# Performance work log

Hardware: AMD Instinct MI355X
Metric: run time of the kernel (lower is better)

## Reference

```python
import jax, jax.numpy as jnp
import numpy as np

B, L, D = 16, 1024, 768

def setup_inputs() -> dict:
    key = jax.random.key(0)
    k1, k2, k3, k4 = jax.random.split(key, 4)
    d_embedding = jax.random.normal(k1, (B, L, D), dtype=jnp.float32)
    d_mask = jax.random.randint(k2, (B, L), 0, 2) == 1
    W = jax.random.normal(k3, (D, D), dtype=jnp.float32) / np.sqrt(D)
    b = jax.random.normal(k4, (D,), dtype=jnp.float32) * 0.01
    return {"d_embedding": d_embedding, "d_mask": d_mask, "W": W, "b": b}

def reference(d_embedding, d_mask, W, b):
    # linear + relu projection: [B, L, D]
    p = jax.nn.relu(jnp.einsum('bld,de->ble', d_embedding, W.T) + b)
    # self-attention scores: [B, L, L]
    scores = jnp.einsum('bld,bmd->blm', p, p)
    # zero out the diagonal (multiply by (1 - eye))
    diag_off = 1.0 - jnp.eye(L, dtype=scores.dtype)
    scores = scores * diag_off[None, :, :]
    # mask padded key positions with -inf (columns)
    scores = jnp.where(d_mask[:, None, :], -jnp.inf, scores)
    # softmax over keys
    alpha = jax.nn.softmax(scores, axis=-1)  # [B, L, L]
    align_feature = jnp.einsum('blm,bmd->bld', alpha, d_embedding)
    return align_feature, alpha
```

## Files before the change

### kernel.cpp

```cpp
#include <hip/hip_runtime.h>
#include <math.h>

#define B_ 16
#define L_ 1024
#define D_ 768

typedef short bf16x8 __attribute__((ext_vector_type(8)));
typedef _Float16 half8 __attribute__((ext_vector_type(8)));
typedef float f32x4 __attribute__((ext_vector_type(4)));

__device__ __forceinline__ unsigned short f2bf(float x) {
  unsigned u = __float_as_uint(x);
  u = (u + 0x7FFFu + ((u >> 16) & 1u)) >> 16;
  return (unsigned short)u;
}
__device__ __forceinline__ float bf2f(unsigned short h) {
  return __uint_as_float(((unsigned)h) << 16);
}
__device__ __forceinline__ unsigned short f2h(float x) {
  union { _Float16 h; unsigned short u; } v;
  v.h = (_Float16)x;
  return v.u;
}

__global__ __launch_bounds__(256) void k_mask2(const void* __restrict__ mraw,
                                               int* __restrict__ canon,
                                               int* __restrict__ psum,
                                               int* __restrict__ kinfo) {
  __shared__ int flags[2];
  __shared__ int tsum[256];
  const int b = blockIdx.x;
  const int tid = threadIdx.x;
  if (tid < 2) flags[tid] = 0;
  __syncthreads();
  const unsigned* m32 = (const unsigned*)mraw;
  int gt = 0, oddnz = 0;
  for (int i = tid; i < 4096; i += 256) {
    unsigned v = m32[i];
    if (v > 1u) gt = 1;
    if ((i & 1) && v != 0u) oddnz = 1;
  }
  if (gt) atomicOr(&flags[0], 1);
  if (oddnz) atomicOr(&flags[1], 1);
  __syncthreads();
  const int mode = flags[0] ? 0 : (flags[1] ? 1 : 2);
  int v[4];
#pragma unroll
  for (int e = 0; e < 4; ++e) {
    const int i = b * L_ + tid * 4 + e;
    int mv;
    if (mode == 0)      mv = ((const unsigned char*)mraw)[i];
    else if (mode == 1) mv = ((const int*)mraw)[i];
    else                mv = (int)(((const long long*)mraw)[i] != 0);
    v[e] = (mv != 0);
    canon[i] = v[e];
  }
  const int vc = (1 - v[0]) + (1 - v[1]) + (1 - v[2]) + (1 - v[3]);
  tsum[tid] = vc;
  __syncthreads();
  for (int off = 1; off < 256; off <<= 1) {
    const int t = (tid >= off) ? tsum[tid - off] : 0;
    __syncthreads();
    tsum[tid] += t;
    __syncthreads();
  }
  int run = tsum[tid] - vc;
#pragma unroll
  for (int e = 0; e < 4; ++e) {
    psum[b * L_ + tid * 4 + e] = run;
    run += 1 - v[e];
  }
  if (tid == 255) {
    const int tot = tsum[255];
    kinfo[b] = (tot + 63) >> 6;
    kinfo[16 + b] = tot;
  }
}

__global__ __launch_bounds__(256) void k_prep16(const float* __restrict__ X,
                                                unsigned short* __restrict__ Xf,
                                                unsigned short* __restrict__ Xt,
                                                const int* __restrict__ psum,
                                                const int* __restrict__ canon,
                                                const int* __restrict__ kinfo) {
  __shared__ unsigned short t16[64][66];
  const int b = blockIdx.z;
  const int d0 = blockIdx.x * 64, m0 = blockIdx.y * 64;
  const int dd = threadIdx.x & 63, mq = threadIdx.x >> 6;
#pragma unroll
  for (int i = 0; i < 16; ++i) {
    const int m = mq * 16 + i;
    const size_t gidx = ((size_t)b * L_ + m0 + m) * D_ + d0 + dd;
    const unsigned short h = f2h(X[gidx]);
    Xf[gidx] = h;
    t16[dd][m] = h;
  }
  __syncthreads();
  const int mm = threadIdx.x & 63, dq = threadIdx.x >> 6;
  const int gm = m0 + mm;
  if (!canon[b * L_ + gm]) {
    const int j = psum[b * L_ + gm];
#pragma unroll
    for (int i = 0; i < 16; ++i) {
      const int d = dq * 16 + i;
      Xt[((size_t)b * D_ + d0 + d) * L_ + j] = t16[d][mm];
    }
  }
  if (blockIdx.y == 15) {
    const int nt64 = kinfo[b] * 64;
    const int kv = kinfo[16 + b];
    if (kv < nt64) {
      const int rr = threadIdx.x >> 2, cg = threadIdx.x & 3;
      unsigned short* base = Xt + ((size_t)b * D_ + d0 + rr) * L_;
#pragma unroll
      for (int q = 0; q < 16; ++q) {
        const int c = kv + cg * 16 + q;
        if (c < nt64) base[c] = 0;
      }
    }
  }
}

__global__ __launch_bounds__(256) void k_prep(const float* __restrict__ X,
                                              unsigned short* __restrict__ Xh,
                                              unsigned short* __restrict__ Xl,
                                              unsigned short* __restrict__ Xt) {
  __shared__ unsigned short t16[64][66];
  const int b = blockIdx.z;
  const int d0 = blockIdx.x * 64, m0 = blockIdx.y * 64;
  const int dd = threadIdx.x & 63, mq = threadIdx.x >> 6;
#pragma unroll
  for (int i = 0; i < 16; ++i) {
    const int m = mq * 16 + i;
    const size_t gidx = ((size_t)b * L_ + m0 + m) * D_ + d0 + dd;
    const float x = X[gidx];
    const unsigned short h = f2bf(x);
    Xh[gidx] = h;
    Xl[gidx] = f2bf(x - bf2f(h));
    t16[dd][m] = h;
  }
  __syncthreads();
  const int mm = threadIdx.x & 63, dq = threadIdx.x >> 6;
#pragma unroll
  for (int i = 0; i < 16; ++i) {
    const int d = dq * 16 + i;
    Xt[((size_t)b * D_ + d0 + d) * L_ + m0 + mm] = t16[d][mm];
  }
}

__global__ __launch_bounds__(256) void k_castW(const float* __restrict__ W,
                                               unsigned short* __restrict__ Wf,
                                               int n8) {
  const int i = blockIdx.x * 256 + threadIdx.x;
  if (i >= n8) return;
  const float4 a = *(const float4*)(W + (size_t)i * 8);
  const float4 b = *(const float4*)(W + (size_t)i * 8 + 4);
  *(ushort4*)(Wf + (size_t)i * 8)     = make_ushort4(f2h(a.x), f2h(a.y), f2h(a.z), f2h(a.w));
  *(ushort4*)(Wf + (size_t)i * 8 + 4) = make_ushort4(f2h(b.x), f2h(b.y), f2h(b.z), f2h(b.w));
}

__device__ __forceinline__ void stage_panel(const unsigned short* __restrict__ ph,
                                            const unsigned short* __restrict__ pl,
                                            size_t grow0, int kk,
                                            char* ldsbase, int wave, int lane) {
#pragma unroll
  for (int q = 0; q < 4; ++q) {
    const int s = wave * 4 + q;
    const int row = s * 8 + (lane >> 3);
    const int xs = (lane & 7) ^ (row & 7);
    const unsigned short* src = (xs & 4) ? pl : ph;
    const unsigned short* g = src + (grow0 + row) * D_ + kk + (xs & 3) * 8;
    __builtin_amdgcn_global_load_lds(
        (const __attribute__((address_space(1))) void*)g,
        (__attribute__((address_space(3))) void*)(ldsbase + s * 1024),
        16, 0, 0);
  }
}

__device__ __forceinline__ void stage_panel1(const unsigned short* __restrict__ g0,
                                             size_t rstride,
                                             char* ldsbase, int wave, int lane) {
#pragma unroll
  for (int q = 0; q < 4; ++q) {
    const int s = wave * 4 + q;
    const int row = s * 8 + (lane >> 3);
    const int xs = (lane & 7) ^ (row & 7);
    const unsigned short* g = g0 + (size_t)row * rstride + xs * 8;
    __builtin_amdgcn_global_load_lds(
        (const __attribute__((address_space(1))) void*)g,
        (__attribute__((address_space(3))) void*)(ldsbase + s * 1024),
        16, 0, 0);
  }
}

__device__ __forceinline__ bf16x8 ldsfrag(const char* base, int row, int g) {
  return *(const bf16x8*)(base + row * 128 + ((g ^ (row & 7)) * 16));
}
__device__ __forceinline__ half8 ldsfrag_h(const char* base, int row, int g) {
  return *(const half8*)(base + row * 128 + ((g ^ (row & 7)) * 16));
}

__global__ __launch_bounds__(256) void k_proj3(const unsigned short* __restrict__ Xf,
                                               const unsigned short* __restrict__ Wf,
                                               const float* __restrict__ bias,
                                               unsigned short* __restrict__ Pf) {
  __shared__ __align__(16) char smem[49152];
  const int tid = threadIdx.x;
  const int xcd = (int)blockIdx.x & 7;
  const int li  = (int)blockIdx.x >> 3;
  const int m0 = (xcd * 16 + li / 6) * 128;
  const int n0 = (li % 6) * 128;
  const int lane = tid & 63, wave = tid >> 6;
  const int wr = wave >> 1, wc = wave & 1;
  const int fr = lane & 15, kg = lane >> 4;
  f32x4 acc[4][4];
#pragma unroll
  for (int i = 0; i < 4; ++i)
#pragma unroll
    for (int j = 0; j < 4; ++j) acc[i][j] = 0;

  const unsigned short* a0 = Xf + (size_t)m0 * D_;
  const unsigned short* b0 = Wf + (size_t)n0 * D_;

  stage_panel1(a0, D_, smem, wave, lane);
  stage_panel1(b0, D_, smem + 32768, wave, lane);
  __syncthreads();

  int cur = 0;
  for (int it = 0; it < D_ / 64; ++it) {
    const char* ab = smem + cur * 16384;
    const char* bb = smem + 32768;
    half8 fa[2][4], fb[2][4];
#pragma unroll
    for (int i = 0; i < 4; ++i) {
      const int ra = wr * 64 + i * 16 + fr;
      const int rb = wc * 64 + i * 16 + fr;
#pragma unroll
      for (int ks = 0; ks < 2; ++ks) {
        fa[ks][i] = ldsfrag_h(ab, ra, ks * 4 + kg);
        fb[ks][i] = ldsfrag_h(bb, rb, ks * 4 + kg);
      }
    }
    __syncthreads();
    if (it + 1 < D_ / 64) {
      stage_panel1(a0 + (it + 1) * 64, D_, smem + (cur ^ 1) * 16384, wave, lane);
      stage_panel1(b0 + (it + 1) * 64, D_, smem + 32768, wave, lane);
    }
#pragma unroll
    for (int ks = 0; ks < 2; ++ks)
#pragma unroll
      for (int i = 0; i < 4; ++i)
#pragma unroll
        for (int j = 0; j < 4; ++j)
          acc[i][j] = __builtin_amdgcn_mfma_f32_16x16x32_f16(fa[ks][i], fb[ks][j],
                                                             acc[i][j], 0, 0, 0);
    __syncthreads();
    cur ^= 1;
  }

  unsigned short* scr = (unsigned short*)smem + wave * 1152;
  const int row = lane >> 2, seg = lane & 3;
  float bj[4];
#pragma unroll
  for (int j = 0; j < 4; ++j) bj[j] = bias[n0 + wc * 64 + j * 16 + fr];
  for (int i = 0; i < 4; ++i) {
    __syncthreads();
#pragma unroll
    for (int j = 0; j < 4; ++j)
#pragma unroll
      for (int r = 0; r < 4; ++r)
        scr[(kg * 4 + r) * 72 + j * 16 + fr] = f2h(fmaxf(acc[i][j][r] + bj[j], 0.f));
    __syncthreads();
    const size_t gr = (size_t)(m0 + wr * 64 + i * 16 + row);
    const int gc0 = n0 + wc * 64 + seg * 16;
    const uint4 h0 = *(const uint4*)&scr[row * 72 + seg * 16];
    const uint4 h1 = *(const uint4*)&scr[row * 72 + seg * 16 + 8];
    *(uint4*)(Pf + gr * D_ + gc0)     = h0;
    *(uint4*)(Pf + gr * D_ + gc0 + 8) = h1;
  }
}

__global__ __launch_bounds__(256) void k_proj(const float* __restrict__ X,
                                              const float* __restrict__ W,
                                              const float* __restrict__ bias,
                                              unsigned short* __restrict__ Ph,
                                              unsigned short* __restrict__ Pl) {
  __shared__ __align__(16) unsigned short smem[4 * 128 * 32];
  unsigned short (*Ah)[32] = (unsigned short(*)[32])smem;
  unsigned short (*Al)[32] = (unsigned short(*)[32])(smem + 1 * 128 * 32);
  unsigned short (*Bh)[32] = (unsigned short(*)[32])(smem + 2 * 128 * 32);
  unsigned short (*Bl)[32] = (unsigned short(*)[32])(smem + 3 * 128 * 32);

  const int tid = threadIdx.x;
  const int swz = ((int)blockIdx.x % 8) * 96 + (int)blockIdx.x / 8;
  const int m0 = (swz / 6) * 128, n0 = (swz % 6) * 128;
  const int lane = tid & 63, wave = tid >> 6;
  const int wr = wave >> 1, wc = wave & 1;
  const int fr = lane & 15, kg = lane >> 4;
  f32x4 acc[4][4];
#pragma unroll
  for (int i = 0; i < 4; ++i)
#pragma unroll
    for (int j = 0; j < 4; ++j) acc[i][j] = 0;

  float4 av[4], bv[4];
#pragma unroll
  for (int p = 0; p < 4; ++p) {
    const int f = tid + p * 256, r = f >> 3, c = f & 7;
    av[p] = *(const float4*)(X + (size_t)(m0 + r) * D_ + c * 4);
    bv[p] = *(const float4*)(W + (size_t)(n0 + r) * D_ + c * 4);
  }

  for (int it = 0; it < D_ / 32; ++it) {
    __syncthreads();
#pragma unroll
    for (int p = 0; p < 4; ++p) {
      const int f = tid + p * 256, r = f >> 3, c = f & 7;
      {
        const float x0 = av[p].x, x1 = av[p].y, x2 = av[p].z, x3 = av[p].w;
        const unsigned short h0 = f2bf(x0), h1 = f2bf(x1), h2 = f2bf(x2), h3 = f2bf(x3);
        *(ushort4*)&Ah[r][c * 4] = make_ushort4(h0, h1, h2, h3);
        *(ushort4*)&Al[r][c * 4] = make_ushort4(f2bf(x0 - bf2f(h0)), f2bf(x1 - bf2f(h1)),
                                                f2bf(x2 - bf2f(h2)), f2bf(x3 - bf2f(h3)));
      }
      {
        const float x0 = bv[p].x, x1 = bv[p].y, x2 = bv[p].z, x3 = bv[p].w;
        const unsigned short h0 = f2bf(x0), h1 = f2bf(x1), h2 = f2bf(x2), h3 = f2bf(x3);
        *(ushort4*)&Bh[r][c * 4] = make_ushort4(h0, h1, h2, h3);
        *(ushort4*)&Bl[r][c * 4] = make_ushort4(f2bf(x0 - bf2f(h0)), f2bf(x1 - bf2f(h1)),
                                                f2bf(x2 - bf2f(h2)), f2bf(x3 - bf2f(h3)));
      }
    }
    __syncthreads();
    if (it + 1 < D_ / 32) {
      const int kk = (it + 1) * 32;
#pragma unroll
      for (int p = 0; p < 4; ++p) {
        const int f = tid + p * 256, r = f >> 3, c = f & 7;
        av[p] = *(const float4*)(X + (size_t)(m0 + r) * D_ + kk + c * 4);
        bv[p] = *(const float4*)(W + (size_t)(n0 + r) * D_ + kk + c * 4);
      }
    }
    bf16x8 fah[4], fal[4], fbh[4], fbl[4];
#pragma unroll
    for (int i = 0; i < 4; ++i) {
      fah[i] = *(const bf16x8*)&Ah[wr * 64 + i * 16 + fr][kg * 8];
      fal[i] = *(const bf16x8*)&Al[wr * 64 + i * 16 + fr][kg * 8];
      fbh[i] = *(const bf16x8*)&Bh[wc * 64 + i * 16 + fr][kg * 8];
      fbl[i] = *(const bf16x8*)&Bl[wc * 64 + i * 16 + fr][kg * 8];
    }
#pragma unroll
    for (int i = 0; i < 4; ++i)
#pragma unroll
      for (int j = 0; j < 4; ++j) {
        acc[i][j] = __builtin_amdgcn_mfma_f32_16x16x32_bf16(fah[i], fbh[j], acc[i][j], 0, 0, 0);
        acc[i][j] = __builtin_amdgcn_mfma_f32_16x16x32_bf16(fah[i], fbl[j], acc[i][j], 0, 0, 0);
        acc[i][j] = __builtin_amdgcn_mfma_f32_16x16x32_bf16(fal[i], fbh[j], acc[i][j], 0, 0, 0);
      }
  }

  unsigned short* scr = smem + wave * 2304;
  const int row = lane >> 2, seg = lane & 3;
  float bj[4];
#pragma unroll
  for (int j = 0; j < 4; ++j) bj[j] = bias[n0 + wc * 64 + j * 16 + fr];
  for (int i = 0; i < 4; ++i) {
    __syncthreads();
#pragma unroll
    for (int j = 0; j < 4; ++j)
#pragma unroll
      for (int r = 0; r < 4; ++r) {
        float v = fmaxf(acc[i][j][r] + bj[j], 0.f);
        const unsigned short h = f2bf(v);
        scr[(kg * 4 + r) * 72 + j * 16 + fr] = h;
        scr[1152 + (kg * 4 + r) * 72 + j * 16 + fr] = f2bf(v - bf2f(h));
      }
    __syncthreads();
    const size_t gr = (size_t)(m0 + wr * 64 + i * 16 + row);
    const int gc0 = n0 + wc * 64 + seg * 16;
    const uint4 h0 = *(const uint4*)&scr[row * 72 + seg * 16];
    const uint4 h1 = *(const uint4*)&scr[row * 72 + seg * 16 + 8];
    const uint4 q0 = *(const uint4*)&scr[1152 + row * 72 + seg * 16];
    const uint4 q1 = *(const uint4*)&scr[1152 + row * 72 + seg * 16 + 8];
    *(uint4*)(Ph + gr * D_ + gc0)     = h0;
    *(uint4*)(Ph + gr * D_ + gc0 + 8) = h1;
    *(uint4*)(Pl + gr * D_ + gc0)     = q0;
    *(uint4*)(Pl + gr * D_ + gc0 + 8) = q1;
  }
}

__global__ __launch_bounds__(256) void k_scores(const unsigned short* __restrict__ Pf,
                                                const int* __restrict__ mask,
                                                float* __restrict__ S) {
  __shared__ __align__(16) char smem[65536];

  const int tid = threadIdx.x;
  const int swz = ((int)blockIdx.x % 8) * 72 + (int)blockIdx.x / 8;
  const int bb = swz / 36;
  const int pr = swz % 36;
  int ti = 0;
  while ((ti + 1) * (ti + 2) / 2 <= pr) ++ti;
  const int tj = pr - ti * (ti + 1) / 2;
  const int l0 = ti * 128, m0 = tj * 128;
  const int lane = tid & 63, wave = tid >> 6;
  const int wr = wave >> 1, wc = wave & 1;
  const int fr = lane & 15, kg = lane >> 4;
  f32x4 acc[4][4];
#pragma unroll
  for (int i = 0; i < 4; ++i)
#pragma unroll
    for (int j = 0; j < 4; ++j) acc[i][j] = 0;

  const unsigned short* a0 = Pf + ((size_t)bb * L_ + l0) * D_;
  const unsigned short* b0 = Pf + ((size_t)bb * L_ + m0) * D_;

  stage_panel1(a0, D_, smem, wave, lane);
  stage_panel1(b0, D_, smem + 16384, wave, lane);
  __syncthreads();

  int cur = 0;
  for (int it = 0; it < D_ / 64; ++it) {
    char* cb = smem + cur * 32768;
    if (it + 1 < D_ / 64) {
      char* nb = smem + (cur ^ 1) * 32768;
      stage_panel1(a0 + (it + 1) * 64, D_, nb, wave, lane);
      stage_panel1(b0 + (it + 1) * 64, D_, nb + 16384, wave, lane);
    }
    half8 fa[2][4], fb[2][4];
#pragma unroll
    for (int i = 0; i < 4; ++i) {
      const int ra = wr * 64 + i * 16 + fr;
      const int rb = wc * 64 + i * 16 + fr;
#pragma unroll
      for (int ks = 0; ks < 2; ++ks) {
        fa[ks][i] = ldsfrag_h(cb, ra, ks * 4 + kg);
        fb[ks][i] = ldsfrag_h(cb + 16384, rb, ks * 4 + kg);
      }
    }
#pragma unroll
    for (int ks = 0; ks < 2; ++ks)
#pragma unroll
      for (int i = 0; i < 4; ++i)
#pragma unroll
        for (int j = 0; j < 4; ++j)
          acc[i][j] = __builtin_amdgcn_mfma_f32_16x16x32_f16(fa[ks][i], fb[ks][j],
                                                             acc[i][j], 0, 0, 0);
    __syncthreads();
    cur ^= 1;
  }

  float* scr = (float*)smem + wave * 1280;
  const int row = lane >> 2, seg = lane & 3;
  for (int i = 0; i < 4; ++i) {
    __syncthreads();
#pragma unroll
    for (int j = 0; j < 4; ++j)
#pragma unroll
      for (int r = 0; r < 4; ++r)
        scr[(kg * 4 + r) * 68 + j * 16 + fr] = acc[i][j][r];
    __syncthreads();
    const int gl = l0 + wr * 64 + i * 16 + row;
    const int gm0 = m0 + wc * 64 + seg * 16;
    const size_t sbase = ((size_t)bb * L_ + gl) * L_ + gm0;
#pragma unroll
    for (int t = 0; t < 4; ++t) {
      float4 o = *(const float4*)&scr[row * 68 + seg * 16 + t * 4];
      const int4 mk = *(const int4*)(mask + bb * L_ + gm0 + t * 4);
      float* op = (float*)&o;
      const int* mp = (const int*)&mk;
#pragma unroll
      for (int e = 0; e < 4; ++e) {
        const int gm = gm0 + t * 4 + e;
        if (gm == gl) op[e] = 0.f;
        if (mp[e]) op[e] = -INFINITY;
      }
      *(float4*)(S + sbase + t * 4) = o;
    }
  }

  if (ti != tj) {
    __syncthreads();
#pragma unroll
    for (int j = 0; j < 4; ++j) {
      const int mloc = wc * 64 + j * 16 + fr;
#pragma unroll
      for (int i = 0; i < 4; ++i) {
        const int slot = wr * 16 + i * 4 + kg;
        const int xs = slot ^ (mloc & 7);
        *(f32x4*)(smem + mloc * 512 + xs * 16) = acc[i][j];
      }
    }
    __syncthreads();
    const int mrow = tid >> 1, half = tid & 1;
    const size_t sbase = ((size_t)bb * L_ + m0 + mrow) * L_ + l0;
#pragma unroll
    for (int q = 0; q < 16; ++q) {
      const int slot = half * 16 + q;
      const int xs = slot ^ (mrow & 7);
      float4 o = *(const float4*)(smem + mrow * 512 + xs * 16);
      const int4 mk = *(const int4*)(mask + bb * L_ + l0 + slot * 4);
      if (mk.x) o.x = -INFINITY;
      if (mk.y) o.y = -INFINITY;
      if (mk.z) o.z = -INFINITY;
      if (mk.w) o.w = -INFINITY;
      *(float4*)(S + sbase + slot * 4) = o;
    }
  }
}

__global__ __launch_bounds__(256) void k_scores_bf(const unsigned short* __restrict__ Ph,
                                                   const unsigned short* __restrict__ Pl,
                                                   const int* __restrict__ mask,
                                                   float* __restrict__ S) {
  __shared__ __align__(16) char smem[65536];

  const int tid = threadIdx.x;
  const int swz = ((int)blockIdx.x % 8) * 72 + (int)blockIdx.x / 8;
  const int bb = swz / 36;
  const int pr = swz % 36;
  int ti = 0;
  while ((ti + 1) * (ti + 2) / 2 <= pr) ++ti;
  const int tj = pr - ti * (ti + 1) / 2;
  const int l0 = ti * 128, m0 = tj * 128;
  const int lane = tid & 63, wave = tid >> 6;
  const int wr = wave >> 1, wc = wave & 1;
  const int fr = lane & 15, kg = lane >> 4;
  f32x4 acc[4][4];
#pragma unroll
  for (int i = 0; i < 4; ++i)
#pragma unroll
    for (int j = 0; j < 4; ++j) acc[i][j] = 0;

  const size_t arow0 = (size_t)bb * L_ + l0;
  const size_t brow0 = (size_t)bb * L_ + m0;

  stage_panel(Ph, Pl, arow0, 0, smem, wave, lane);
  stage_panel(Ph, Pl, brow0, 0, smem + 16384, wave, lane);
  __syncthreads();

  int cur = 0;
  for (int it = 0; it < D_ / 32; ++it) {
    char* cb = smem + cur * 32768;
    if (it + 1 < D_ / 32) {
      char* nb = smem + (cur ^ 1) * 32768;
      stage_panel(Ph, Pl, arow0, (it + 1) * 32, nb, wave, lane);
      stage_panel(Ph, Pl, brow0, (it + 1) * 32, nb + 16384, wave, lane);
    }
    bf16x8 fah[4], fal[4], fbh[4], fbl[4];
#pragma unroll
    for (int i = 0; i < 4; ++i) {
      const int ra = wr * 64 + i * 16 + fr;
      const int rb = wc * 64 + i * 16 + fr;
      fah[i] = ldsfrag(cb, ra, kg);
      fal[i] = ldsfrag(cb, ra, kg + 4);
      fbh[i] = ldsfrag(cb + 16384, rb, kg);
      fbl[i] = ldsfrag(cb + 16384, rb, kg + 4);
    }
#pragma unroll
    for (int i = 0; i < 4; ++i)
#pragma unroll
      for (int j = 0; j < 4; ++j) {
        acc[i][j] = __builtin_amdgcn_mfma_f32_16x16x32_bf16(fah[i], fbh[j], acc[i][j], 0, 0, 0);
        acc[i][j] = __builtin_amdgcn_mfma_f32_16x16x32_bf16(fah[i], fbl[j], acc[i][j], 0, 0, 0);
        acc[i][j] = __builtin_amdgcn_mfma_f32_16x16x32_bf16(fal[i], fbh[j], acc[i][j], 0, 0, 0);
      }
    __syncthreads();
    cur ^= 1;
  }

  float* scr = (float*)smem + wave * 1280;
  const int row = lane >> 2, seg = lane & 3;
  for (int i = 0; i < 4; ++i) {
    __syncthreads();
#pragma unroll
    for (int j = 0; j < 4; ++j)
#pragma unroll
      for (int r = 0; r < 4; ++r)
        scr[(kg * 4 + r) * 68 + j * 16 + fr] = acc[i][j][r];
    __syncthreads();
    const int gl = l0 + wr * 64 + i * 16 + row;
    const int gm0 = m0 + wc * 64 + seg * 16;
    const size_t sbase = ((size_t)bb * L_ + gl) * L_ + gm0;
#pragma unroll
    for (int t = 0; t < 4; ++t) {
      float4 o = *(const float4*)&scr[row * 68 + seg * 16 + t * 4];
      const int4 mk = *(const int4*)(mask + bb * L_ + gm0 + t * 4);
      float* op = (float*)&o;
      const int* mp = (const int*)&mk;
#pragma unroll
      for (int e = 0; e < 4; ++e) {
        const int gm = gm0 + t * 4 + e;
        if (gm == gl) op[e] = 0.f;
        if (mp[e]) op[e] = -INFINITY;
      }
      *(float4*)(S + sbase + t * 4) = o;
    }
  }

  if (ti != tj) {
    __syncthreads();
#pragma unroll
    for (int j = 0; j < 4; ++j) {
      const int mloc = wc * 64 + j * 16 + fr;
#pragma unroll
      for (int i = 0; i < 4; ++i) {
        const int slot = wr * 16 + i * 4 + kg;
        const int xs = slot ^ (mloc & 7);
        *(f32x4*)(smem + mloc * 512 + xs * 16) = acc[i][j];
      }
    }
    __syncthreads();
    const int mrow = tid >> 1, half = tid & 1;
    const size_t sbase = ((size_t)bb * L_ + m0 + mrow) * L_ + l0;
#pragma unroll
    for (int q = 0; q < 16; ++q) {
      const int slot = half * 16 + q;
      const int xs = slot ^ (mrow & 7);
      float4 o = *(const float4*)(smem + mrow * 512 + xs * 16);
      const int4 mk = *(const int4*)(mask + bb * L_ + l0 + slot * 4);
      if (mk.x) o.x = -INFINITY;
      if (mk.y) o.y = -INFINITY;
      if (mk.z) o.z = -INFINITY;
      if (mk.w) o.w = -INFINITY;
      *(float4*)(S + sbase + slot * 4) = o;
    }
  }
}

__global__ __launch_bounds__(256) void k_softmax(float* __restrict__ S,
                                                 unsigned short* __restrict__ a16,
                                                 const int* __restrict__ psum,
                                                 const int* __restrict__ canon,
                                                 const int* __restrict__ kinfo) {
  const size_t row = blockIdx.x;
  float4* rp = (float4*)(S + row * L_);
  float4 v = rp[threadIdx.x];
  float mx = fmaxf(fmaxf(v.x, v.y), fmaxf(v.z, v.w));
#pragma unroll
  for (int o = 32; o > 0; o >>= 1) mx = fmaxf(mx, __shfl_xor(mx, o));
  __shared__ float rmax[4], rsum[4];
  const int wv = threadIdx.x >> 6, ln = threadIdx.x & 63;
  if (ln == 0) rmax[wv] = mx;
  __syncthreads();
  mx = fmaxf(fmaxf(rmax[0], rmax[1]), fmaxf(rmax[2], rmax[3]));
  float4 e;
  e.x = __expf(v.x - mx); e.y = __expf(v.y - mx);
  e.z = __expf(v.z - mx); e.w = __expf(v.w - mx);
  float s = (e.x + e.y) + (e.z + e.w);
#pragma unroll
  for (int o = 32; o > 0; o >>= 1) s += __shfl_xor(s, o);
  if (ln == 0) rsum[wv] = s;
  __syncthreads();
  s = (rsum[0] + rsum[1]) + (rsum[2] + rsum[3]);
  const float inv = 1.0f / s;
  e.x *= inv; e.y *= inv; e.z *= inv; e.w *= inv;
  rp[threadIdx.x] = e;
  if (a16) {
    const int bbat = (int)(row >> 10);
    const int m0 = threadIdx.x * 4;
    const int4 mk = *(const int4*)(canon + bbat * L_ + m0);
    const int4 ps = *(const int4*)(psum + bbat * L_ + m0);
    unsigned short* arow = a16 + row * L_;
    if (!mk.x) arow[ps.x] = f2h(e.x);
    if (!mk.y) arow[ps.y] = f2h(e.y);
    if (!mk.z) arow[ps.z] = f2h(e.z);
    if (!mk.w) arow[ps.w] = f2h(e.w);
    const int nt64 = kinfo[bbat] * 64;
    const int kv = kinfo[16 + bbat];
    const int c = kv + (int)threadIdx.x;
    if (c < nt64) arow[c] = 0;
  }
}

__global__ __launch_bounds__(256) void k_align2(const unsigned short* __restrict__ A16,
                                                const unsigned short* __restrict__ Xt,
                                                const int* __restrict__ kinfo,
                                                float* __restrict__ O) {
  __shared__ __align__(16) char smem[49152];
  const int tid = threadIdx.x;
  const int swz = ((int)blockIdx.x % 8) * 96 + (int)blockIdx.x / 8;
  const int bb = swz / 48;
  const int l0 = ((swz / 6) % 8) * 128;
  const int n0 = (swz % 6) * 128;
  const int nt = kinfo[bb];
  const int lane = tid & 63, wave = tid >> 6;
  const int wr = wave >> 1, wc = wave & 1;
  const int fr = lane & 15, kg = lane >> 4;
  f32x4 acc[4][4];
#pragma unroll
  for (int i = 0; i < 4; ++i)
#pragma unroll
    for (int j = 0; j < 4; ++j) acc[i][j] = 0;

  const unsigned short* a0 = A16 + ((size_t)bb * L_ + l0) * L_;
  const unsigned short* b0 = Xt + ((size_t)bb * D_ + n0) * L_;

  if (nt > 0) {
    stage_panel1(a0, L_, smem, wave, lane);
    stage_panel1(b0, L_, smem + 32768, wave, lane);
  }
  __syncthreads();

  int cur = 0;
  for (int it = 0; it < nt; ++it) {
    const char* ab = smem + cur * 16384;
    const char* bb2 = smem + 32768;
    half8 fa[2][4], fb[2][4];
#pragma unroll
    for (int i = 0; i < 4; ++i) {
      const int ra = wr * 64 + i * 16 + fr;
      const int rb = wc * 64 + i * 16 + fr;
#pragma unroll
      for (int ks = 0; ks < 2; ++ks) {
        fa[ks][i] = ldsfrag_h(ab, ra, ks * 4 + kg);
        fb[ks][i] = ldsfrag_h(bb2, rb, ks * 4 + kg);
      }
    }
    __syncthreads();
    if (it + 1 < nt) {
      stage_panel1(a0 + (it + 1) * 64, L_, smem + (cur ^ 1) * 16384, wave, lane);
      stage_panel1(b0 + (it + 1) * 64, L_, smem + 32768, wave, lane);
    }
#pragma unroll
    for (int ks = 0; ks < 2; ++ks)
#pragma unroll
      for (int i = 0; i < 4; ++i)
#pragma unroll
        for (int j = 0; j < 4; ++j)
          acc[i][j] = __builtin_amdgcn_mfma_f32_16x16x32_f16(fa[ks][i], fb[ks][j],
                                                             acc[i][j], 0, 0, 0);
    __syncthreads();
    cur ^= 1;
  }

  float* scr = (float*)smem + wave * 1280;
  const int row = lane >> 2, seg = lane & 3;
  for (int i = 0; i < 4; ++i) {
    __syncthreads();
#pragma unroll
    for (int j = 0; j < 4; ++j)
#pragma unroll
      for (int r = 0; r < 4; ++r)
        scr[(kg * 4 + r) * 68 + j * 16 + fr] = acc[i][j][r];
    __syncthreads();
    const int gl = l0 + wr * 64 + i * 16 + row;
    const int gc0 = n0 + wc * 64 + seg * 16;
    const size_t obase = ((size_t)bb * L_ + gl) * D_ + gc0;
#pragma unroll
    for (int t = 0; t < 4; ++t) {
      const float4 o = *(const float4*)&scr[row * 68 + seg * 16 + t * 4];
      *(float4*)(O + obase + t * 4) = o;
    }
  }
}

__global__ __launch_bounds__(256) void k_align(const float* __restrict__ A,
                                               const unsigned short* __restrict__ Xt,
                                               float* __restrict__ O) {
  __shared__ __align__(16) unsigned short smem[2 * 128 * 32];
  __shared__ __align__(16) float scr_s[4 * 1104];
  unsigned short (*Ab)[32] = (unsigned short(*)[32])smem;
  unsigned short (*Bb)[32] = (unsigned short(*)[32])(smem + 128 * 32);

  const int tid = threadIdx.x;
  const int swz = ((int)blockIdx.x % 8) * 96 + (int)blockIdx.x / 8;
  const int bb = swz / 48;
  const int l0 = ((swz / 6) % 8) * 128;
  const int n0 = (swz % 6) * 128;
  const int lane = tid & 63, wave = tid >> 6;
  const int wr = wave >> 1, wc = wave & 1;
  const int fr = lane & 15, kg = lane >> 4;
  f32x4 acc[4][4];
#pragma unroll
  for (int i = 0; i < 4; ++i)
#pragma unroll
    for (int j = 0; j < 4; ++j) acc[i][j] = 0;

  float4 av[4];
  uint4 bv[2];
#pragma unroll
  for (int p = 0; p < 4; ++p) {
    const int f = tid + p * 256, r = f >> 3, c = f & 7;
    av[p] = *(const float4*)(A + ((size_t)bb * L_ + l0 + r) * L_ + c * 4);
  }
#pragma unroll
  for (int p = 0; p < 2; ++p) {
    const int f = tid + p * 256, r = f >> 2, sl = f & 3;
    bv[p] = *(const uint4*)(Xt + ((size_t)bb * D_ + n0 + r) * L_ + sl * 8);
  }

  for (int it = 0; it < L_ / 32; ++it) {
    __syncthreads();
#pragma unroll
    for (int p = 0; p < 4; ++p) {
      const int f = tid + p * 256, r = f >> 3, c = f & 7;
      *(ushort4*)&Ab[r][c * 4] = make_ushort4(f2bf(av[p].x), f2bf(av[p].y),
                                              f2bf(av[p].z), f2bf(av[p].w));
    }
#pragma unroll
    for (int p = 0; p < 2; ++p) {
      const int f = tid + p * 256, r = f >> 2, sl = f & 3;
      *(uint4*)&Bb[r][sl * 8] = bv[p];
    }
    __syncthreads();
    if (it + 1 < L_ / 32) {
      const int kk = (it + 1) * 32;
#pragma unroll
      for (int p = 0; p < 4; ++p) {
        const int f = tid + p * 256, r = f >> 3, c = f & 7;
        av[p] = *(const float4*)(A + ((size_t)bb * L_ + l0 + r) * L_ + kk + c * 4);
      }
#pragma unroll
      for (int p = 0; p < 2; ++p) {
        const int f = tid + p * 256, r = f >> 2, sl = f & 3;
        bv[p] = *(const uint4*)(Xt + ((size_t)bb * D_ + n0 + r) * L_ + kk + sl * 8);
      }
    }
    bf16x8 fa[4], fb[4];
#pragma unroll
    for (int i = 0; i < 4; ++i) {
      fa[i] = *(const bf16x8*)&Ab[wr * 64 + i * 16 + fr][kg * 8];
      fb[i] = *(const bf16x8*)&Bb[wc * 64 + i * 16 + fr][kg * 8];
    }
#pragma unroll
    for (int i = 0; i < 4; ++i)
#pragma unroll
      for (int j = 0; j < 4; ++j)
        acc[i][j] = __builtin_amdgcn_mfma_f32_16x16x32_bf16(fa[i], fb[j], acc[i][j], 0, 0, 0);
  }

  float* scr = scr_s + wave * 1104;
  const int row = lane >> 2, seg = lane & 3;
  for (int i = 0; i < 4; ++i) {
    __syncthreads();
#pragma unroll
    for (int j = 0; j < 4; ++j)
#pragma unroll
      for (int r = 0; r < 4; ++r)
        scr[(kg * 4 + r) * 68 + j * 16 + fr] = acc[i][j][r];
    __syncthreads();
    const int gl = l0 + wr * 64 + i * 16 + row;
    const int gc0 = n0 + wc * 64 + seg * 16;
    const size_t obase = ((size_t)bb * L_ + gl) * D_ + gc0;
#pragma unroll
    for (int t = 0; t < 4; ++t) {
      const float4 o = *(const float4*)&scr[row * 68 + seg * 16 + t * 4];
      *(float4*)(O + obase + t * 4) = o;
    }
  }
}

extern "C" void kernel_launch(void* const* d_in, const int* in_sizes, int n_in,
                              void* d_out, int out_size, void* d_ws, size_t ws_size,
                              hipStream_t stream) {
  const float* X    = (const float*)d_in[0];
  const void*  mraw = d_in[1];
  const float* W    = (const float*)d_in[2];
  const float* bias = (const float*)d_in[3];

  float* out   = (float*)d_out;
  float* align = out;
  float* alpha = out + (size_t)B_ * L_ * D_;

  const size_t NX = (size_t)B_ * L_ * D_;
  const size_t NW = (size_t)D_ * D_;
  const size_t NA = (size_t)B_ * L_ * L_;

  int* maskC = (int*)d_ws;
  int* psum  = (int*)((char*)d_ws + 65536);
  int* kinfo = (int*)((char*)d_ws + 131072);
  const size_t offXt = 135168;
  unsigned short* Xt = (unsigned short*)((char*)d_ws + offXt);
  const size_t offWf = offXt + NX * 2;
  const size_t offA16 = offWf;
  const size_t need = offA16 + NA * 2;

  hipLaunchKernelGGL(k_mask2, dim3(16), dim3(256), 0, stream, mraw, maskC, psum, kinfo);

  if (ws_size >= need) {
    unsigned short* Xf = (unsigned short*)alpha;
    unsigned short* Wf = (unsigned short*)((char*)d_ws + offWf);
    unsigned short* Pf = (unsigned short*)align;
    unsigned short* A16 = (unsigned short*)((char*)d_ws + offA16);
    hipLaunchKernelGGL(k_prep16, dim3(D_ / 64, L_ / 64, B_), dim3(256), 0, stream,
                       X, Xf, Xt, psum, maskC, kinfo);
    hipLaunchKernelGGL(k_castW, dim3((int)(NW / 8 / 256)), dim3(256), 0, stream,
                       W, Wf, (int)(NW / 8));
    hipLaunchKernelGGL(k_proj3, dim3(768), dim3(256), 0, stream, Xf, Wf, bias, Pf);
    hipLaunchKernelGGL(k_scores, dim3(576), dim3(256), 0, stream, Pf, maskC, alpha);
    hipLaunchKernelGGL(k_softmax, dim3(B_ * L_), dim3(256), 0, stream,
                       alpha, A16, psum, maskC, kinfo);
    hipLaunchKernelGGL(k_align2, dim3(768), dim3(256), 0, stream, A16, Xt, kinfo, align);
  } else {
    unsigned short* Ph = (unsigned short*)align;
    unsigned short* Pl = Ph + NX;
    hipLaunchKernelGGL(k_prep, dim3(D_ / 64, L_ / 64, B_), dim3(256), 0, stream,
                       X, (unsigned short*)alpha, (unsigned short*)alpha + NX, Xt);
    hipLaunchKernelGGL(k_proj, dim3(768), dim3(256), 0, stream, X, W, bias, Ph, Pl);
    hipLaunchKernelGGL(k_scores_bf, dim3(576), dim3(256), 0, stream, Ph, Pl, maskC, alpha);
    hipLaunchKernelGGL(k_softmax, dim3(B_ * L_), dim3(256), 0, stream,
                       alpha, (unsigned short*)nullptr, psum, maskC, kinfo);
    hipLaunchKernelGGL(k_align, dim3(768), dim3(256), 0, stream, alpha, Xt, align);
  }
}
```

Measured before the change: 162.4 us.

## Compute scores only over compacted non-padded keys and scatter in softmax

```diff
diff --git a/kernel.cpp b/kernel.cpp
--- a/kernel.cpp
+++ b/kernel.cpp
@@ -26,7 +26,8 @@
 __global__ __launch_bounds__(256) void k_mask2(const void* __restrict__ mraw,
                                                int* __restrict__ canon,
                                                int* __restrict__ psum,
-                                               int* __restrict__ kinfo) {
+                                               int* __restrict__ kinfo,
+                                               int* __restrict__ ctok) {
   __shared__ int flags[2];
   __shared__ int tsum[256];
   const int b = blockIdx.x;
@@ -54,6 +55,7 @@
     else                mv = (int)(((const long long*)mraw)[i] != 0);
     v[e] = (mv != 0);
     canon[i] = v[e];
+    ctok[i] = 0;
   }
   const int vc = (1 - v[0]) + (1 - v[1]) + (1 - v[2]) + (1 - v[3]);
   tsum[tid] = vc;
@@ -68,6 +70,7 @@
 #pragma unroll
   for (int e = 0; e < 4; ++e) {
     psum[b * L_ + tid * 4 + e] = run;
+    if (!v[e]) ctok[b * L_ + run] = tid * 4 + e;
     run += 1 - v[e];
   }
   if (tid == 255) {
@@ -186,6 +189,22 @@
     const int row = s * 8 + (lane >> 3);
     const int xs = (lane & 7) ^ (row & 7);
     const unsigned short* g = g0 + (size_t)row * rstride + xs * 8;
+    __builtin_amdgcn_global_load_lds(
+        (const __attribute__((address_space(1))) void*)g,
+        (__attribute__((address_space(3))) void*)(ldsbase + s * 1024),
+        16, 0, 0);
+  }
+}
+
+__device__ __forceinline__ void stage_panelI(const unsigned short* __restrict__ base,
+                                             const int* __restrict__ tokB,
+                                             int kk, char* ldsbase, int wave, int lane) {
+#pragma unroll
+  for (int q = 0; q < 4; ++q) {
+    const int s = wave * 4 + q;
+    const int row = s * 8 + (lane >> 3);
+    const int xs = (lane & 7) ^ (row & 7);
+    const unsigned short* g = base + (size_t)tokB[q] * D_ + kk + xs * 8;
     __builtin_amdgcn_global_load_lds(
         (const __attribute__((address_space(1))) void*)g,
         (__attribute__((address_space(3))) void*)(ldsbase + s * 1024),
@@ -389,9 +408,103 @@
   }
 }
 
-__global__ __launch_bounds__(256) void k_scores(const unsigned short* __restrict__ Pf,
-                                                const int* __restrict__ mask,
-                                                float* __restrict__ S) {
+__global__ __launch_bounds__(256) void k_scores_c(const unsigned short* __restrict__ Pf,
+                                                  const int* __restrict__ ctok,
+                                                  const int* __restrict__ kinfo,
+                                                  float* __restrict__ S) {
+  __shared__ __align__(16) char smem[49152];
+  const int tid = threadIdx.x;
+  const int swz = ((int)blockIdx.x & 7) * 128 + ((int)blockIdx.x >> 3);
+  const int bb = swz >> 6;
+  const int l0 = ((swz >> 3) & 7) * 128;
+  const int c0 = (swz & 7) * 128;
+  const int kv = kinfo[16 + bb];
+  if (c0 >= kv) return;
+
+  const int lane = tid & 63, wave = tid >> 6;
+  const int wr = wave >> 1, wc = wave & 1;
+  const int fr = lane & 15, kg = lane >> 4;
+  f32x4 acc[4][4];
+#pragma unroll
+  for (int i = 0; i < 4; ++i)
+#pragma unroll
+    for (int j = 0; j < 4; ++j) acc[i][j] = 0;
+
+  const unsigned short* Pfb = Pf + (size_t)bb * L_ * D_;
+  const int* ctokb = ctok + bb * L_;
+  const unsigned short* a0 = Pfb + (size_t)l0 * D_;
+
+  int tokB[4];
+#pragma unroll
+  for (int q = 0; q < 4; ++q)
+    tokB[q] = ctokb[c0 + (wave * 4 + q) * 8 + (lane >> 3)];
+
+  stage_panel1(a0, D_, smem, wave, lane);
+  stage_panelI(Pfb, tokB, 0, smem + 32768, wave, lane);
+  __syncthreads();
+
+  int cur = 0;
+  for (int it = 0; it < D_ / 64; ++it) {
+    const char* ab = smem + cur * 16384;
+    const char* bpan = smem + 32768;
+    half8 fa[2][4], fb[2][4];
+#pragma unroll
+    for (int i = 0; i < 4; ++i) {
+      const int ra = wr * 64 + i * 16 + fr;
+      const int rb = wc * 64 + i * 16 + fr;
+#pragma unroll
+      for (int ks = 0; ks < 2; ++ks) {
+        fa[ks][i] = ldsfrag_h(ab, ra, ks * 4 + kg);
+        fb[ks][i] = ldsfrag_h(bpan, rb, ks * 4 + kg);
+      }
+    }
+    __syncthreads();
+    if (it + 1 < D_ / 64) {
+      stage_panel1(a0 + (it + 1) * 64, D_, smem + (cur ^ 1) * 16384, wave, lane);
+      stage_panelI(Pfb, tokB, (it + 1) * 64, smem + 32768, wave, lane);
+    }
+#pragma unroll
+    for (int ks = 0; ks < 2; ++ks)
+#pragma unroll
+      for (int i = 0; i < 4; ++i)
+#pragma unroll
+        for (int j = 0; j < 4; ++j)
+          acc[i][j] = __builtin_amdgcn_mfma_f32_16x16x32_f16(fa[ks][i], fb[ks][j],
+                                                             acc[i][j], 0, 0, 0);
+    __syncthreads();
+    cur ^= 1;
+  }
+
+  float* scr = (float*)smem + wave * 1280;
+  const int row = lane >> 2, seg = lane & 3;
+  for (int i = 0; i < 4; ++i) {
+    __syncthreads();
+#pragma unroll
+    for (int j = 0; j < 4; ++j)
+#pragma unroll
+      for (int r = 0; r < 4; ++r)
+        scr[(kg * 4 + r) * 68 + j * 16 + fr] = acc[i][j][r];
+    __syncthreads();
+    const int gl = l0 + wr * 64 + i * 16 + row;
+    const int gcb = c0 + wc * 64 + seg * 16;
+    const size_t sbase = ((size_t)bb * L_ + gl) * L_ + gcb;
+#pragma unroll
+    for (int t = 0; t < 4; ++t) {
+      float4 o = *(const float4*)&scr[row * 68 + seg * 16 + t * 4];
+      const int4 tk = *(const int4*)(ctokb + gcb + t * 4);
+      if (tk.x == gl) o.x = 0.f;
+      if (tk.y == gl) o.y = 0.f;
+      if (tk.z == gl) o.z = 0.f;
+      if (tk.w == gl) o.w = 0.f;
+      *(float4*)(S + sbase + t * 4) = o;
+    }
+  }
+}
+
+__global__ __launch_bounds__(256) void k_scores_bf(const unsigned short* __restrict__ Ph,
+                                                   const unsigned short* __restrict__ Pl,
+                                                   const int* __restrict__ mask,
+                                                   float* __restrict__ S) {
   __shared__ __align__(16) char smem[65536];
 
   const int tid = threadIdx.x;
@@ -411,40 +524,39 @@
 #pragma unroll
     for (int j = 0; j < 4; ++j) acc[i][j] = 0;
 
-  const unsigned short* a0 = Pf + ((size_t)bb * L_ + l0) * D_;
-  const unsigned short* b0 = Pf + ((size_t)bb * L_ + m0) * D_;
-
-  stage_panel1(a0, D_, smem, wave, lane);
-  stage_panel1(b0, D_, smem + 16384, wave, lane);
+  const size_t arow0 = (size_t)bb * L_ + l0;
+  const size_t brow0 = (size_t)bb * L_ + m0;
+
+  stage_panel(Ph, Pl, arow0, 0, smem, wave, lane);
+  stage_panel(Ph, Pl, brow0, 0, smem + 16384, wave, lane);
   __syncthreads();
 
   int cur = 0;
-  for (int it = 0; it < D_ / 64; ++it) {
+  for (int it = 0; it < D_ / 32; ++it) {
     char* cb = smem + cur * 32768;
-    if (it + 1 < D_ / 64) {
+    if (it + 1 < D_ / 32) {
       char* nb = smem + (cur ^ 1) * 32768;
-      stage_panel1(a0 + (it + 1) * 64, D_, nb, wave, lane);
-      stage_panel1(b0 + (it + 1) * 64, D_, nb + 16384, wave, lane);
-    }
-    half8 fa[2][4], fb[2][4];
+      stage_panel(Ph, Pl, arow0, (it + 1) * 32, nb, wave, lane);
+      stage_panel(Ph, Pl, brow0, (it + 1) * 32, nb + 16384, wave, lane);
+    }
+    bf16x8 fah[4], fal[4], fbh[4], fbl[4];
 #pragma unroll
     for (int i = 0; i < 4; ++i) {
       const int ra = wr * 64 + i * 16 + fr;
       const int rb = wc * 64 + i * 16 + fr;
-#pragma unroll
-      for (int ks = 0; ks < 2; ++ks) {
-        fa[ks][i] = ldsfrag_h(cb, ra, ks * 4 + kg);
-        fb[ks][i] = ldsfrag_h(cb + 16384, rb, ks * 4 + kg);
-      }
-    }
-#pragma unroll
-    for (int ks = 0; ks < 2; ++ks)
-#pragma unroll
-      for (int i = 0; i < 4; ++i)
-#pragma unroll
-        for (int j = 0; j < 4; ++j)
-          acc[i][j] = __builtin_amdgcn_mfma_f32_16x16x32_f16(fa[ks][i], fb[ks][j],
-                                                             acc[i][j], 0, 0, 0);
+      fah[i] = ldsfrag(cb, ra, kg);
+      fal[i] = ldsfrag(cb, ra, kg + 4);
+      fbh[i] = ldsfrag(cb + 16384, rb, kg);
+      fbl[i] = ldsfrag(cb + 16384, rb, kg + 4);
+    }
+#pragma unroll
+    for (int i = 0; i < 4; ++i)
+#pragma unroll
+      for (int j = 0; j < 4; ++j) {
+        acc[i][j] = __builtin_amdgcn_mfma_f32_16x16x32_bf16(fah[i], fbh[j], acc[i][j], 0, 0, 0);
+        acc[i][j] = __builtin_amdgcn_mfma_f32_16x16x32_bf16(fah[i], fbl[j], acc[i][j], 0, 0, 0);
+        acc[i][j] = __builtin_amdgcn_mfma_f32_16x16x32_bf16(fal[i], fbh[j], acc[i][j], 0, 0, 0);
+      }
     __syncthreads();
     cur ^= 1;
   }
@@ -508,130 +620,68 @@
   }
 }
 
-__global__ __launch_bounds__(256) void k_scores_bf(const unsigned short* __restrict__ Ph,
-                                                   const unsigned short* __restrict__ Pl,
-                                                   const int* __restrict__ mask,
-                                                   float* __restrict__ S) {
-  __shared__ __align__(16) char smem[65536];
-
+__global__ __launch_bounds__(256) void k_softmax_c(float* __restrict__ S,
+                                                   unsigned short* __restrict__ a16,
+                                                   const int* __restrict__ ctok,
+                                                   const int* __restrict__ kinfo) {
+  __shared__ float ar[1024];
+  __shared__ float rmax[4], rsum[4];
+  const size_t row = blockIdx.x;
+  const int bb = (int)(row >> 10);
+  const int kv = kinfo[16 + bb];
+  const int nt64 = kinfo[bb] * 64;
   const int tid = threadIdx.x;
-  const int swz = ((int)blockIdx.x % 8) * 72 + (int)blockIdx.x / 8;
-  const int bb = swz / 36;
-  const int pr = swz % 36;
-  int ti = 0;
-  while ((ti + 1) * (ti + 2) / 2 <= pr) ++ti;
-  const int tj = pr - ti * (ti + 1) / 2;
-  const int l0 = ti * 128, m0 = tj * 128;
-  const int lane = tid & 63, wave = tid >> 6;
-  const int wr = wave >> 1, wc = wave & 1;
-  const int fr = lane & 15, kg = lane >> 4;
-  f32x4 acc[4][4];
-#pragma unroll
-  for (int i = 0; i < 4; ++i)
-#pragma unroll
-    for (int j = 0; j < 4; ++j) acc[i][j] = 0;
-
-  const size_t arow0 = (size_t)bb * L_ + l0;
-  const size_t brow0 = (size_t)bb * L_ + m0;
-
-  stage_panel(Ph, Pl, arow0, 0, smem, wave, lane);
-  stage_panel(Ph, Pl, brow0, 0, smem + 16384, wave, lane);
-  __syncthreads();
-
-  int cur = 0;
-  for (int it = 0; it < D_ / 32; ++it) {
-    char* cb = smem + cur * 32768;
-    if (it + 1 < D_ / 32) {
-      char* nb = smem + (cur ^ 1) * 32768;
-      stage_panel(Ph, Pl, arow0, (it + 1) * 32, nb, wave, lane);
-      stage_panel(Ph, Pl, brow0, (it + 1) * 32, nb + 16384, wave, lane);
-    }
-    bf16x8 fah[4], fal[4], fbh[4], fbl[4];
-#pragma unroll
-    for (int i = 0; i < 4; ++i) {
-      const int ra = wr * 64 + i * 16 + fr;
-      const int rb = wc * 64 + i * 16 + fr;
-      fah[i] = ldsfrag(cb, ra, kg);
-      fal[i] = ldsfrag(cb, ra, kg + 4);
-      fbh[i] = ldsfrag(cb + 16384, rb, kg);
-      fbl[i] = ldsfrag(cb + 16384, rb, kg + 4);
-    }
-#pragma unroll
-    for (int i = 0; i < 4; ++i)
-#pragma unroll
-      for (int j = 0; j < 4; ++j) {
-        acc[i][j] = __builtin_amdgcn_mfma_f32_16x16x32_bf16(fah[i], fbh[j], acc[i][j], 0, 0, 0);
-        acc[i][j] = __builtin_amdgcn_mfma_f32_16x16x32_bf16(fah[i], fbl[j], acc[i][j], 0, 0, 0);
-        acc[i][j] = __builtin_amdgcn_mfma_f32_16x16x32_bf16(fal[i], fbh[j], acc[i][j], 0, 0, 0);
-      }
-    __syncthreads();
-    cur ^= 1;
-  }
-
-  float* scr = (float*)smem + wave * 1280;
-  const int row = lane >> 2, seg = lane & 3;
-  for (int i = 0; i < 4; ++i) {
-    __syncthreads();
-#pragma unroll
-    for (int j = 0; j < 4; ++j)
-#pragma unroll
-      for (int r = 0; r < 4; ++r)
-        scr[(kg * 4 + r) * 68 + j * 16 + fr] = acc[i][j][r];
-    __syncthreads();
-    const int gl = l0 + wr * 64 + i * 16 + row;
-    const int gm0 = m0 + wc * 64 + seg * 16;
-    const size_t sbase = ((size_t)bb * L_ + gl) * L_ + gm0;
-#pragma unroll
-    for (int t = 0; t < 4; ++t) {
-      float4 o = *(const float4*)&scr[row * 68 + seg * 16 + t * 4];
-      const int4 mk = *(const int4*)(mask + bb * L_ + gm0 + t * 4);
-      float* op = (float*)&o;
-      const int* mp = (const int*)&mk;
-#pragma unroll
-      for (int e = 0; e < 4; ++e) {
-        const int gm = gm0 + t * 4 + e;
-        if (gm == gl) op[e] = 0.f;
-        if (mp[e]) op[e] = -INFINITY;
-      }
-      *(float4*)(S + sbase + t * 4) = o;
-    }
-  }
-
-  if (ti != tj) {
-    __syncthreads();
-#pragma unroll
-    for (int j = 0; j < 4; ++j) {
-      const int mloc = wc * 64 + j * 16 + fr;
-#pragma unroll
-      for (int i = 0; i < 4; ++i) {
-        const int slot = wr * 16 + i * 4 + kg;
-        const int xs = slot ^ (mloc & 7);
-        *(f32x4*)(smem + mloc * 512 + xs * 16) = acc[i][j];
-      }
-    }
-    __syncthreads();
-    const int mrow = tid >> 1, half = tid & 1;
-    const size_t sbase = ((size_t)bb * L_ + m0 + mrow) * L_ + l0;
-#pragma unroll
-    for (int q = 0; q < 16; ++q) {
-      const int slot = half * 16 + q;
-      const int xs = slot ^ (mrow & 7);
-      float4 o = *(const float4*)(smem + mrow * 512 + xs * 16);
-      const int4 mk = *(const int4*)(mask + bb * L_ + l0 + slot * 4);
-      if (mk.x) o.x = -INFINITY;
-      if (mk.y) o.y = -INFINITY;
-      if (mk.z) o.z = -INFINITY;
-      if (mk.w) o.w = -INFINITY;
-      *(float4*)(S + sbase + slot * 4) = o;
-    }
-  }
-}
-
-__global__ __launch_bounds__(256) void k_softmax(float* __restrict__ S,
-                                                 unsigned short* __restrict__ a16,
-                                                 const int* __restrict__ psum,
-                                                 const int* __restrict__ canon,
-                                                 const int* __restrict__ kinfo) {
+  const int p0 = tid * 4;
+
+  const float4 v = *(const float4*)(S + row * L_ + p0);
+  float vv[4];
+#pragma unroll
+  for (int e = 0; e < 4; ++e) vv[e] = (p0 + e < kv) ? ((const float*)&v)[e] : -INFINITY;
+
+  float mx = fmaxf(fmaxf(vv[0], vv[1]), fmaxf(vv[2], vv[3]));
+#pragma unroll
+  for (int o = 32; o > 0; o >>= 1) mx = fmaxf(mx, __shfl_xor(mx, o));
+  const int wv = tid >> 6, ln = tid & 63;
+  if (ln == 0) rmax[wv] = mx;
+  __syncthreads();
+  mx = fmaxf(fmaxf(rmax[0], rmax[1]), fmaxf(rmax[2], rmax[3]));
+
+  float ee[4];
+  float s = 0.f;
+#pragma unroll
+  for (int e = 0; e < 4; ++e) {
+    ee[e] = (p0 + e < kv) ? __expf(vv[e] - mx) : 0.f;
+    s += ee[e];
+  }
+#pragma unroll
+  for (int o = 32; o > 0; o >>= 1) s += __shfl_xor(s, o);
+  if (ln == 0) rsum[wv] = s;
+  __syncthreads();
+  s = (rsum[0] + rsum[1]) + (rsum[2] + rsum[3]);
+  const float inv = 1.0f / s;
+#pragma unroll
+  for (int e = 0; e < 4; ++e) ee[e] *= inv;
+
+  if (p0 < nt64) {
+    ushort4 h;
+    h.x = (p0 + 0 < kv) ? f2h(ee[0]) : 0;
+    h.y = (p0 + 1 < kv) ? f2h(ee[1]) : 0;
+    h.z = (p0 + 2 < kv) ? f2h(ee[2]) : 0;
+    h.w = (p0 + 3 < kv) ? f2h(ee[3]) : 0;
+    *(ushort4*)(a16 + row * L_ + p0) = h;
+  }
+
+  *(float4*)&ar[p0] = make_float4(0.f, 0.f, 0.f, 0.f);
+  __syncthreads();
+  const int* ctokb = ctok + bb * L_;
+#pragma unroll
+  for (int e = 0; e < 4; ++e)
+    if (p0 + e < kv) ar[ctokb[p0 + e]] = ee[e];
+  __syncthreads();
+  *(float4*)(S + row * L_ + p0) = *(const float4*)&ar[p0];
+}
+
+__global__ __launch_bounds__(256) void k_softmax(float* __restrict__ S) {
   const size_t row = blockIdx.x;
   float4* rp = (float4*)(S + row * L_);
   float4 v = rp[threadIdx.x];
@@ -655,21 +705,6 @@
   const float inv = 1.0f / s;
   e.x *= inv; e.y *= inv; e.z *= inv; e.w *= inv;
   rp[threadIdx.x] = e;
-  if (a16) {
-    const int bbat = (int)(row >> 10);
-    const int m0 = threadIdx.x * 4;
-    const int4 mk = *(const int4*)(canon + bbat * L_ + m0);
-    const int4 ps = *(const int4*)(psum + bbat * L_ + m0);
-    unsigned short* arow = a16 + row * L_;
-    if (!mk.x) arow[ps.x] = f2h(e.x);
-    if (!mk.y) arow[ps.y] = f2h(e.y);
-    if (!mk.z) arow[ps.z] = f2h(e.z);
-    if (!mk.w) arow[ps.w] = f2h(e.w);
-    const int nt64 = kinfo[bbat] * 64;
-    const int kv = kinfo[16 + bbat];
-    const int c = kv + (int)threadIdx.x;
-    if (c < nt64) arow[c] = 0;
-  }
 }
 
 __global__ __launch_bounds__(256) void k_align2(const unsigned short* __restrict__ A16,
@@ -869,13 +904,14 @@
   int* maskC = (int*)d_ws;
   int* psum  = (int*)((char*)d_ws + 65536);
   int* kinfo = (int*)((char*)d_ws + 131072);
-  const size_t offXt = 135168;
+  int* ctok  = (int*)((char*)d_ws + 135168);
+  const size_t offXt = 135168 + 65536;
   unsigned short* Xt = (unsigned short*)((char*)d_ws + offXt);
   const size_t offWf = offXt + NX * 2;
   const size_t offA16 = offWf;
   const size_t need = offA16 + NA * 2;
 
-  hipLaunchKernelGGL(k_mask2, dim3(16), dim3(256), 0, stream, mraw, maskC, psum, kinfo);
+  hipLaunchKernelGGL(k_mask2, dim3(16), dim3(256), 0, stream, mraw, maskC, psum, kinfo, ctok);
 
   if (ws_size >= need) {
     unsigned short* Xf = (unsigned short*)alpha;
@@ -887,9 +923,9 @@
     hipLaunchKernelGGL(k_castW, dim3((int)(NW / 8 / 256)), dim3(256), 0, stream,
                        W, Wf, (int)(NW / 8));
     hipLaunchKernelGGL(k_proj3, dim3(768), dim3(256), 0, stream, Xf, Wf, bias, Pf);
-    hipLaunchKernelGGL(k_scores, dim3(576), dim3(256), 0, stream, Pf, maskC, alpha);
-    hipLaunchKernelGGL(k_softmax, dim3(B_ * L_), dim3(256), 0, stream,
-                       alpha, A16, psum, maskC, kinfo);
+    hipLaunchKernelGGL(k_scores_c, dim3(1024), dim3(256), 0, stream, Pf, ctok, kinfo, alpha);
+    hipLaunchKernelGGL(k_softmax_c, dim3(B_ * L_), dim3(256), 0, stream,
+                       alpha, A16, ctok, kinfo);
     hipLaunchKernelGGL(k_align2, dim3(768), dim3(256), 0, stream, A16, Xt, kinfo, align);
   } else {
     unsigned short* Ph = (unsigned short*)align;
@@ -898,8 +934,7 @@
                        X, (unsigned short*)alpha, (unsigned short*)alpha + NX, Xt);
     hipLaunchKernelGGL(k_proj, dim3(768), dim3(256), 0, stream, X, W, bias, Ph, Pl);
     hipLaunchKernelGGL(k_scores_bf, dim3(576), dim3(256), 0, stream, Ph, Pl, maskC, alpha);
-    hipLaunchKernelGGL(k_softmax, dim3(B_ * L_), dim3(256), 0, stream,
-                       alpha, (unsigned short*)nullptr, psum, maskC, kinfo);
+    hipLaunchKernelGGL(k_softmax, dim3(B_ * L_), dim3(256), 0, stream, alpha);
     hipLaunchKernelGGL(k_align, dim3(768), dim3(256), 0, stream, alpha, Xt, align);
   }
 }
```

New measurement: 159.9 us. About the same (-1.6%).
